# Optimization experiments

Hardware: AMD Instinct MI355X
Metric: run time of the kernel (lower is better)

## Reference

```python
import jax, jax.numpy as jnp
import numpy as np

N_QUBITS = 6
N_LAYERS = 2
QSVT_DEGREE = 3
DT_RANK = max(N_QUBITS // 2, 1)
OUT_DIM = 3 * N_QUBITS
PI = np.float32(np.pi)
DT_MIN, DT_MAX = 1e-3, 0.1
BATCH, SEQ = 256, 512


def _ry_mat(theta):
    c = jnp.cos(theta / 2)
    s = jnp.sin(theta / 2)
    row0 = jnp.stack([c, -s], axis=-1)
    row1 = jnp.stack([s, c], axis=-1)
    return jnp.stack([row0, row1], axis=-2).astype(jnp.complex64)


def _rz_mat(theta):
    e = jnp.exp(-0.5j * theta.astype(jnp.complex64))
    z = jnp.zeros_like(e)
    row0 = jnp.stack([e, z], axis=-1)
    row1 = jnp.stack([z, jnp.conj(e)], axis=-1)
    return jnp.stack([row0, row1], axis=-2)


def _rx_mat(theta):
    c = jnp.cos(theta / 2).astype(jnp.complex64)
    s = jnp.sin(theta / 2).astype(jnp.complex64)
    row0 = jnp.stack([c, -1j * s], axis=-1)
    row1 = jnp.stack([-1j * s, c], axis=-1)
    return jnp.stack([row0, row1], axis=-2)


def _apply1(state, mat, w):
    # state: (B, 2, ..., 2) tensor over N_QUBITS axes; mat: (2,2) or batched (B,2,2)
    state = jnp.moveaxis(state, 1 + w, -1)
    if mat.ndim == 3:
        state = jnp.einsum('bij,b...j->b...i', mat, state)
    else:
        state = jnp.einsum('ij,b...j->b...i', mat, state)
    return jnp.moveaxis(state, -1, 1 + w)


def _cnot(state, c, t):
    state = jnp.moveaxis(state, (1 + c, 1 + t), (-2, -1))
    state = state.at[..., 1, :].set(state[..., 1, ::-1])
    return jnp.moveaxis(state, (-2, -1), (1 + c, 1 + t))


def _crx(state, theta, c, t):
    state = jnp.moveaxis(state, (1 + c, 1 + t), (-2, -1))
    m = _rx_mat(theta)
    state = state.at[..., 1, :].set(jnp.einsum('ij,...j->...i', m, state[..., 1, :]))
    return jnp.moveaxis(state, (-2, -1), (1 + c, 1 + t))


def _circuit(h, x, dt, circuit_params, poly_coeffs, qsvt_params):
    """Batched statevector simulation of the selective QSVT + unified ansatz qnode."""
    n = N_QUBITS
    B = h.shape[0]
    state = jnp.zeros((B,) + (2,) * n, jnp.complex64)
    state = state.at[(slice(None),) + (0,) * n].set(1.0 + 0.0j)
    # 1) state encoding RY(h[t-1])
    for i in range(n):
        state = _apply1(state, _ry_mat(h[:, i]), i)
    # 2) Delta-modulated QSVT: RZ rotations + bidirectional CNOT ring per degree
    qidx = 0
    n_qp = n * QSVT_DEGREE
    for deg in range(QSVT_DEGREE + 1):
        coeff = poly_coeffs[deg]
        for i in range(n):
            if qidx < n_qp:
                ang = coeff * dt[:, i] * qsvt_params[qidx] * PI
                qidx += 1
            else:
                ang = coeff * dt[:, i] * PI
            state = _apply1(state, _rz_mat(ang), i)
        for i in range(n - 1):
            state = _cnot(state, i, i + 1)
        state = _cnot(state, n - 1, 0)
        for i in range(n - 1, 0, -1):
            state = _cnot(state, i, i - 1)
    # 3) unified variational ansatz
    p = 0
    for _ in range(N_LAYERS):
        for i in range(n):
            state = _apply1(state, _rx_mat(circuit_params[p]), i)
            state = _apply1(state, _ry_mat(circuit_params[p + 1]), i)
            state = _apply1(state, _rz_mat(circuit_params[p + 2]), i)
            p += 3
        for i in range(n):
            state = _crx(state, circuit_params[p], i, (i + 1) % n)
            p += 1
        for i in range(n - 1, -1, -1):
            state = _crx(state, circuit_params[p], i, (i - 1) % n)
            p += 1
    # 4) Delta-modulated input RY(x * dt)
    for i in range(n):
        state = _apply1(state, _ry_mat(x[:, i] * dt[:, i]), i)
    # 5) Pauli X/Y/Z expectation values per qubit
    xs, ys, zs = [], [], []
    for i in range(n):
        s = jnp.moveaxis(state, 1 + i, 1).reshape(B, 2, -1)
        z = jnp.sum(jnp.conj(s[:, 0]) * s[:, 1], axis=-1)
        xs.append(2.0 * jnp.real(z))
        ys.append(2.0 * jnp.imag(z))
        zs.append(jnp.sum(jnp.abs(s[:, 0]) ** 2 - jnp.abs(s[:, 1]) ** 2, axis=-1))
    return jnp.stack(xs + ys + zs, axis=-1).astype(jnp.float32)  # (B, 3n)


def setup_inputs() -> dict:
    key = jax.random.key(0)
    ks = jax.random.split(key, 8)
    angles = jax.random.uniform(ks[0], (BATCH, SEQ, N_QUBITS), jnp.float32) * PI
    Wx = jax.random.normal(ks[1], (DT_RANK + 2 * N_QUBITS, N_QUBITS), jnp.float32) / np.float32(np.sqrt(N_QUBITS))
    Wdt = jax.random.normal(ks[2], (N_QUBITS, DT_RANK), jnp.float32) / np.float32(np.sqrt(DT_RANK))
    dt = jnp.exp(jax.random.uniform(ks[3], (N_QUBITS,), jnp.float32) * np.float32(np.log(DT_MAX) - np.log(DT_MIN)) + np.float32(np.log(DT_MIN)))
    bdt = dt + jnp.log(-jnp.expm1(-dt))
    poly_coeffs = jax.random.normal(ks[4], (QSVT_DEGREE + 1,), jnp.float32) * 0.1
    qsvt_params = jax.random.normal(ks[5], (N_QUBITS * QSVT_DEGREE,), jnp.float32) * 0.1
    circuit_params = jax.random.normal(ks[6], (5 * N_QUBITS * N_LAYERS,), jnp.float32) * 0.1
    D = jnp.ones((OUT_DIM,), jnp.float32)
    Wc = jax.random.normal(ks[7], (OUT_DIM, N_QUBITS), jnp.float32) / np.float32(np.sqrt(N_QUBITS))
    return {"angles": angles, "Wx": Wx, "Wdt": Wdt, "bdt": bdt, "poly_coeffs": poly_coeffs, "qsvt_params": qsvt_params, "circuit_params": circuit_params, "D": D, "Wc": Wc}


def reference(angles, Wx, Wdt, bdt, poly_coeffs, qsvt_params, circuit_params, D, Wc):
    x_dbc = angles @ Wx.T  # (B,S, dt_rank + 2n)
    dt_raw = x_dbc[..., :DT_RANK]
    # B slice computed in the original but never used in forward
    C = x_dbc[..., DT_RANK + N_QUBITS:]
    dt_angles = jnp.tanh(jax.nn.softplus(dt_raw @ Wdt.T + bdt)) * PI  # (B,S,n)
    # quantum part is detached in the original (detach().cpu() before the qnode)
    sg = jax.lax.stop_gradient
    xs = (jnp.moveaxis(sg(angles), 1, 0), jnp.moveaxis(sg(dt_angles), 1, 0))
    cp, pc, qp = sg(circuit_params), sg(poly_coeffs), sg(qsvt_params)
    h0 = jnp.zeros((angles.shape[0], N_QUBITS), jnp.float32)

    def step(h, xt):
        x_t, dt_t = xt
        meas = _circuit(h, x_t, dt_t, cp, pc, qp)
        return meas[:, 2 * N_QUBITS:], meas  # carry = PauliZ block

    _, meas = jax.lax.scan(step, h0, xs)
    h_full = jnp.moveaxis(meas, 0, 1)  # (B,S,3n)
    return (C @ Wc.T) * h_full + D * jnp.concatenate([angles] * 3, axis=-1)
```

## Files before the change

### kernel.cpp

```cpp
#include <hip/hip_runtime.h>
#include <math.h>

#define BATCH 256
#define SEQ 512
#define SDS 54
#define PI_F 3.14159265358979323846f

template<int CTRL>
__device__ __forceinline__ float fdpp(float v) {
    return __int_as_float(__builtin_amdgcn_mov_dpp(__float_as_int(v), CTRL, 0xF, 0xF, true));
}
template<int L>
__device__ __forceinline__ float rdl(float v) {
    return __int_as_float(__builtin_amdgcn_readlane(__float_as_int(v), L));
}
__device__ __forceinline__ float rdlv(float v, int l) {
    return __int_as_float(__builtin_amdgcn_readlane(__float_as_int(v), l));
}
template<int M>
__device__ __forceinline__ float shxm(float v) {
    if constexpr (M == 1)       return fdpp<0xB1>(v);
    else if constexpr (M == 2)  return fdpp<0x4E>(v);
    else if constexpr (M == 8)  return fdpp<0x128>(v);
    else if constexpr (M == 32) return __shfl_xor(v, 32, 64);
    else return __int_as_float(__builtin_amdgcn_ds_swizzle(__float_as_int(v), (M << 10) | 0x1F));
}
__device__ __forceinline__ float redsum64(float v) {
    v += fdpp<0x128>(v);
    v += fdpp<0x124>(v);
    v += fdpp<0x122>(v);
    v += fdpp<0x121>(v);
    return (rdl<0>(v) + rdl<16>(v)) + (rdl<32>(v) + rdl<48>(v));
}
__device__ __forceinline__ float xorf(float v, int m) {
    return __int_as_float(__float_as_int(v) ^ m);
}
__device__ __forceinline__ void wg_barrier_lds() {
    __builtin_amdgcn_sched_barrier(0);
    __builtin_amdgcn_s_waitcnt(0xC07F);
    __builtin_amdgcn_s_barrier();
    __builtin_amdgcn_sched_barrier(0);
}
__device__ __forceinline__ int permf(int x) {
    const int cs[11] = {0,1,2,3,4,5,5,4,3,2,1};
    const int ts[11] = {1,2,3,4,5,0,4,3,2,1,0};
#pragma unroll
    for (int k = 10; k >= 0; k--) {
        int cb = (x >> (5 - cs[k])) & 1;
        x ^= cb << (5 - ts[k]);
    }
    return x;
}
__device__ __forceinline__ void cmul4(const float* c,
    float vr, float vi, float ar, float ai, float br, float bi, float cr, float ci,
    float& nr, float& ni) {
    nr = c[0]*vr - c[1]*vi + c[2]*ar - c[3]*ai + c[4]*br - c[5]*bi + c[6]*cr - c[7]*ci;
    ni = c[0]*vi + c[1]*vr + c[2]*ai + c[3]*ar + c[4]*bi + c[5]*br + c[6]*ci + c[7]*cr;
}
__device__ __forceinline__ void ringapply(const float* rc,
    float vr, float vi, float br, float bi, float cr, float ci, float dr, float di,
    float& nr, float& ni) {
    nr = rc[0]*vr - rc[1]*bi - rc[2]*ci + rc[3]*dr;
    ni = rc[0]*vi + rc[1]*br + rc[2]*cr + rc[3]*di;
}

__global__ __launch_bounds__(256) void prep_kernel(
    const float* __restrict__ angles, const float* __restrict__ Wx,
    const float* __restrict__ Wdt, const float* __restrict__ bdt,
    const float* __restrict__ D, const float* __restrict__ Wc,
    float* __restrict__ sd)
{
    int gid = blockIdx.x * blockDim.x + threadIdx.x;
    if (gid >= BATCH * SEQ) return;
    const float* a = angles + (size_t)gid * 6;
    float ang[6];
#pragma unroll
    for (int i = 0; i < 6; i++) ang[i] = a[i];
    float dtr[3];
#pragma unroll
    for (int r = 0; r < 3; r++) {
        float s = 0.f;
#pragma unroll
        for (int k = 0; k < 6; k++) s += ang[k] * Wx[r * 6 + k];
        dtr[r] = s;
    }
    float* rec = sd + (size_t)gid * SDS;
    float dtv[6];
#pragma unroll
    for (int i = 0; i < 6; i++) {
        float x = bdt[i];
#pragma unroll
        for (int r = 0; r < 3; r++) x += dtr[r] * Wdt[i * 3 + r];
        float sp = (x > 15.f) ? x : log1pf(expf(x));
        dtv[i] = tanhf(sp) * PI_F;
        rec[i] = dtv[i];
        float th = ang[i] * dtv[i];
        rec[6 + i]  = cosf(th);
        rec[12 + i] = sinf(th);
    }
    float C[6];
#pragma unroll
    for (int i = 0; i < 6; i++) {
        float s = 0.f;
#pragma unroll
        for (int k = 0; k < 6; k++) s += ang[k] * Wx[(9 + i) * 6 + k];
        C[i] = s;
    }
#pragma unroll
    for (int j = 0; j < 18; j++) {
        float s = 0.f;
#pragma unroll
        for (int i = 0; i < 6; i++) s += C[i] * Wc[j * 6 + i];
        rec[18 + j] = s;
        rec[36 + j] = D[j] * ang[j % 6];
    }
}

__global__ __launch_bounds__(64) void umat_kernel(const float* __restrict__ cp,
                                                  float2* __restrict__ um)
{
    const int lane = threadIdx.x;
    const int col = blockIdx.x;
    int bitv[6];
#pragma unroll
    for (int i = 0; i < 6; i++) bitv[i] = (lane >> (5 - i)) & 1;

    float qc[2][3][8], rc[2][6][4];
#pragma unroll
    for (int l = 0; l < 2; l++) {
        float g00r[6], g00i[6], g01r[6], g01i[6], g10r[6], g10i[6], g11r[6], g11i[6];
#pragma unroll
        for (int i = 0; i < 6; i++) {
            float ax = cp[l * 30 + i * 3 + 0];
            float ay = cp[l * 30 + i * 3 + 1];
            float az = cp[l * 30 + i * 3 + 2];
            float ca = cosf(0.5f * ax), sa = sinf(0.5f * ax);
            float cb = cosf(0.5f * ay), sb = sinf(0.5f * ay);
            float cg = cosf(0.5f * az), sg = sinf(0.5f * az);
            float m00r = cb * ca, m00i =  sb * sa;
            float m01r = -sb * ca, m01i = -cb * sa;
            float m10r =  sb * ca, m10i = -cb * sa;
            float m11r =  cb * ca, m11i = -sb * sa;
            g00r[i] = cg * m00r + sg * m00i; g00i[i] = cg * m00i - sg * m00r;
            g01r[i] = cg * m01r + sg * m01i; g01i[i] = cg * m01i - sg * m01r;
            g10r[i] = cg * m10r - sg * m10i; g10i[i] = cg * m10i + sg * m10r;
            g11r[i] = cg * m11r - sg * m11i; g11i[i] = cg * m11i + sg * m11r;
        }
#pragma unroll
        for (int pp = 0; pp < 3; pp++) {
            int aq = 2 * pp, bq = 2 * pp + 1;
            float dar = bitv[aq] ? g11r[aq] : g00r[aq], dai = bitv[aq] ? g11i[aq] : g00i[aq];
            float oar = bitv[aq] ? g10r[aq] : g01r[aq], oai = bitv[aq] ? g10i[aq] : g01i[aq];
            float dbr = bitv[bq] ? g11r[bq] : g00r[bq], dbi = bitv[bq] ? g11i[bq] : g00i[bq];
            float obr = bitv[bq] ? g10r[bq] : g01r[bq], obi = bitv[bq] ? g10i[bq] : g01i[bq];
            qc[l][pp][0] = dar * dbr - dai * dbi;  qc[l][pp][1] = dar * dbi + dai * dbr;
            qc[l][pp][2] = oar * dbr - oai * dbi;  qc[l][pp][3] = oar * dbi + oai * dbr;
            qc[l][pp][4] = dar * obr - dai * obi;  qc[l][pp][5] = dar * obi + dai * obr;
            qc[l][pp][6] = oar * obr - oai * obi;  qc[l][pp][7] = oar * obi + oai * obr;
        }
        const int Aq[6] = {0, 2, 4, 5, 3, 1};
        const int Bq[6] = {1, 3, 5, 4, 2, 0};
#pragma unroll
        for (int o = 0; o < 6; o++) {
            float tha = (o < 3) ? cp[l * 30 + 18 + 2 * o]     : cp[l * 30 + 24 + 2 * (o - 3)];
            float thb = (o < 3) ? cp[l * 30 + 18 + 2 * o + 1] : cp[l * 30 + 24 + 2 * (o - 3) + 1];
            float ca = cosf(0.5f * tha), sa = sinf(0.5f * tha);
            float cb = cosf(0.5f * thb), sb = sinf(0.5f * thb);
            int ba = bitv[Aq[o]], bb = bitv[Bq[o]];
            float mx0 = ba ? ca : 1.f, sae = ba ? sa : 0.f;
            float ny0 = bb ? cb : 1.f, sbe = bb ? sb : 0.f;
            rc[l][o][0] = ny0 * mx0; rc[l][o][1] = -ny0 * sae;
            rc[l][o][2] = -mx0 * sbe; rc[l][o][3] = -sae * sbe;
        }
    }

    float re = (lane == col) ? 1.f : 0.f;
    float im = 0.f;
    auto p1q = [&](int mi, int mj, const float* c) {
        float ar = __shfl_xor(re, mi, 64), ai = __shfl_xor(im, mi, 64);
        float br = __shfl_xor(re, mj, 64), bi = __shfl_xor(im, mj, 64);
        float cr = __shfl_xor(re, mi | mj, 64), ci = __shfl_xor(im, mi | mj, 64);
        float nr, ni;
        cmul4(c, re, im, ar, ai, br, bi, cr, ci, nr, ni);
        re = nr; im = ni;
    };
    auto rng = [&](int mb, int mc, const float* c) {
        float br = __shfl_xor(re, mb, 64), bi = __shfl_xor(im, mb, 64);
        float cr = __shfl_xor(re, mc, 64), ci = __shfl_xor(im, mc, 64);
        float dr = __shfl_xor(re, mb | mc, 64), di = __shfl_xor(im, mb | mc, 64);
        float nr, ni;
        ringapply(c, re, im, br, bi, cr, ci, dr, di, nr, ni);
        re = nr; im = ni;
    };
#pragma unroll
    for (int l = 0; l < 2; l++) {
        p1q(32, 16, qc[l][0]);
        p1q(8, 4, qc[l][1]);
        p1q(2, 1, qc[l][2]);
        rng(16, 8, rc[l][0]);
        rng(4, 2, rc[l][1]);
        rng(1, 32, rc[l][2]);
        rng(2, 4, rc[l][3]);
        rng(8, 16, rc[l][4]);
        rng(32, 1, rc[l][5]);
    }
    um[(size_t)lane * 64 + col] = make_float2(re, im);
}

__global__ __launch_bounds__(256, 1) void step_kernel(
    const float* __restrict__ sd, const float* __restrict__ pc,
    const float* __restrict__ qp, const float2* __restrict__ um,
    float* __restrict__ out)
{
    __shared__ float2 sPart[4][64];
    __shared__ __align__(16) float sZXY[20];
    const int tid = threadIdx.x;
    const int wave = tid >> 6;
    const int lane = tid & 63;
    const int b = blockIdx.x;

    int bitv[6];
#pragma unroll
    for (int i = 0; i < 6; i++) bitv[i] = (lane >> (5 - i)) & 1;
    int sflip[6];
#pragma unroll
    for (int q = 0; q < 6; q++) sflip[q] = bitv[q] ? (int)0x80000000 : 0;

    const int jbase = wave * 16;
    float2 row[16];
#pragma unroll
    for (int jj = 0; jj < 16; jj++) row[jj] = um[(size_t)lane * 64 + jbase + jj];

    float A[6], sel[6];
    {
        int x1 = permf(lane), x2 = permf(x1), x3 = permf(x2), x4 = permf(x3);
#pragma unroll
        for (int i = 0; i < 6; i++) {
            float u0 = pc[0] * PI_F * qp[0 * 6 + i];
            float u1 = pc[1] * PI_F * qp[1 * 6 + i];
            float u2 = pc[2] * PI_F * qp[2 * 6 + i];
            float u3 = pc[3] * PI_F;
            float t1 = ((x1 >> (5 - i)) & 1) ? 0.5f : -0.5f;
            float t2 = ((x2 >> (5 - i)) & 1) ? 0.5f : -0.5f;
            float t3 = ((x3 >> (5 - i)) & 1) ? 0.5f : -0.5f;
            float t4 = ((x4 >> (5 - i)) & 1) ? 0.5f : -0.5f;
            A[i] = u3 * t1 + u2 * t2 + u1 * t3 + u0 * t4;
            sel[i] = (float)((x4 >> (5 - i)) & 1);
        }
    }

    const float* sdb = sd + (size_t)b * SEQ * SDS;
    float* outb = out + (size_t)b * SEQ * 18;

    float h0 = 0.f, h1 = 0.f, h2 = 0.f, h3 = 0.f, h4 = 0.f, h5 = 0.f;

    float cd[18], nd[18];
#pragma unroll
    for (int k = 0; k < 18; k++) cd[k] = sdb[k];

    for (int t = 0; t < SEQ; t++) {
        const float* r  = sdb + (size_t)t * SDS;
        const float* rn = sdb + (size_t)((t + 1 < SEQ) ? t + 1 : t) * SDS;
#pragma unroll
        for (int k = 0; k < 18; k++) nd[k] = rn[k];

        float phi = A[0]*cd[0] + A[1]*cd[1] + A[2]*cd[2] + A[3]*cd[3] + A[4]*cd[4] + A[5]*cd[5];
        float sph, cph;
        __sincosf(phi, &sph, &cph);

        float ss0, cc0, ss1, cc1, ss2, cc2, ss3, cc3, ss4, cc4, ss5, cc5;
        __sincosf(0.5f * h0, &ss0, &cc0);
        __sincosf(0.5f * h1, &ss1, &cc1);
        __sincosf(0.5f * h2, &ss2, &cc2);
        __sincosf(0.5f * h3, &ss3, &cc3);
        __sincosf(0.5f * h4, &ss4, &cc4);
        __sincosf(0.5f * h5, &ss5, &cc5);
        float f0 = fmaf(sel[0], ss0 - cc0, cc0);
        float f1 = fmaf(sel[1], ss1 - cc1, cc1);
        float f2 = fmaf(sel[2], ss2 - cc2, cc2);
        float f3 = fmaf(sel[3], ss3 - cc3, cc3);
        float f4 = fmaf(sel[4], ss4 - cc4, cc4);
        float f5 = fmaf(sel[5], ss5 - cc5, cc5);
        float prod = ((f0 * f1) * (f2 * f3)) * (f4 * f5);
        float pr = prod * cph, pi = prod * sph;

        float ar0 = 0.f, ai0 = 0.f, ar1 = 0.f, ai1 = 0.f;
#pragma unroll
        for (int jj = 0; jj < 16; jj += 2) {
            float sr0 = rdlv(pr, jbase + jj);
            float si0 = rdlv(pi, jbase + jj);
            float sr1 = rdlv(pr, jbase + jj + 1);
            float si1 = rdlv(pi, jbase + jj + 1);
            ar0 = fmaf(row[jj].x, sr0, ar0);
            ar0 = fmaf(-row[jj].y, si0, ar0);
            ai0 = fmaf(row[jj].x, si0, ai0);
            ai0 = fmaf(row[jj].y, sr0, ai0);
            ar1 = fmaf(row[jj + 1].x, sr1, ar1);
            ar1 = fmaf(-row[jj + 1].y, si1, ar1);
            ai1 = fmaf(row[jj + 1].x, si1, ai1);
            ai1 = fmaf(row[jj + 1].y, sr1, ai1);
        }
        sPart[wave][lane] = make_float2(ar0 + ar1, ai0 + ai1);
        wg_barrier_lds();
        float2 q0v = sPart[0][lane], q1v = sPart[1][lane];
        float2 q2v = sPart[2][lane], q3v = sPart[3][lane];
        float re = (q0v.x + q1v.x) + (q2v.x + q3v.x);
        float im = (q0v.y + q1v.y) + (q2v.y + q3v.y);

        if (wave == 0) {
            float p = re * re + im * im;
            float Z0 = redsum64(xorf(p, sflip[0]));
            float Z1 = redsum64(xorf(p, sflip[1]));
            float Z2 = redsum64(xorf(p, sflip[2]));
            float Z3 = redsum64(xorf(p, sflip[3]));
            float Z4 = redsum64(xorf(p, sflip[4]));
            float Z5 = redsum64(xorf(p, sflip[5]));
            if (lane == 0) {
                sZXY[0] = Z0; sZXY[1] = Z1; sZXY[2] = Z2;
                sZXY[3] = Z3; sZXY[4] = Z4; sZXY[5] = Z5;
            }
        } else if (wave == 1) {
            float g0r = shxm<32>(re), g0i = shxm<32>(im);
            float g1r = shxm<16>(re), g1i = shxm<16>(im);
            float X0 = redsum64(re * g0r + im * g0i);
            float X1 = redsum64(re * g1r + im * g1i);
            float Y0 = redsum64(xorf(re * g0i - im * g0r, sflip[0]));
            float Y1 = redsum64(xorf(re * g1i - im * g1r, sflip[1]));
            if (lane == 0) { sZXY[6] = X0; sZXY[7] = X1; sZXY[12] = Y0; sZXY[13] = Y1; }
        } else if (wave == 2) {
            float g2r = shxm<8>(re), g2i = shxm<8>(im);
            float g3r = shxm<4>(re), g3i = shxm<4>(im);
            float X2 = redsum64(re * g2r + im * g2i);
            float X3 = redsum64(re * g3r + im * g3i);
            float Y2 = redsum64(xorf(re * g2i - im * g2r, sflip[2]));
            float Y3 = redsum64(xorf(re * g3i - im * g3r, sflip[3]));
            if (lane == 0) { sZXY[8] = X2; sZXY[9] = X3; sZXY[14] = Y2; sZXY[15] = Y3; }
        } else {
            float g4r = shxm<2>(re), g4i = shxm<2>(im);
            float g5r = shxm<1>(re), g5i = shxm<1>(im);
            float X4 = redsum64(re * g4r + im * g4i);
            float X5 = redsum64(re * g5r + im * g5i);
            float Y4 = redsum64(xorf(re * g4i - im * g4r, sflip[4]));
            float Y5 = redsum64(xorf(re * g5i - im * g5r, sflip[5]));
            if (lane == 0) { sZXY[10] = X4; sZXY[11] = X5; sZXY[16] = Y4; sZXY[17] = Y5; }
        }
        wg_barrier_lds();

        float4 v0 = ((const float4*)sZXY)[0];
        float4 v1 = ((const float4*)sZXY)[1];
        float4 v2 = ((const float4*)sZXY)[2];
        float Zv[6] = {v0.x, v0.y, v0.z, v0.w, v1.x, v1.y};
        float Xv[6] = {v1.z, v1.w, v2.x, v2.y, v2.z, v2.w};
        h0 = cd[6]  * Zv[0] - cd[12] * Xv[0];
        h1 = cd[7]  * Zv[1] - cd[13] * Xv[1];
        h2 = cd[8]  * Zv[2] - cd[14] * Xv[2];
        h3 = cd[9]  * Zv[3] - cd[15] * Xv[3];
        h4 = cd[10] * Zv[4] - cd[16] * Xv[4];
        h5 = cd[11] * Zv[5] - cd[17] * Xv[5];

        if (wave == 0 && lane == 0) {
            float* o = outb + (size_t)t * 18;
            float hh[6] = {h0, h1, h2, h3, h4, h5};
#pragma unroll
            for (int q = 0; q < 6; q++) o[12 + q] = fmaf(r[30 + q], hh[q], r[48 + q]);
        }
        if (wave == 3 && lane == 0) {
            float* o = outb + (size_t)t * 18;
#pragma unroll
            for (int q = 0; q < 6; q++) {
                float px = cd[6 + q] * Xv[q] + cd[12 + q] * Zv[q];
                o[q]     = fmaf(r[18 + q], px, r[36 + q]);
                o[6 + q] = fmaf(r[24 + q], sZXY[12 + q], r[42 + q]);
            }
        }

#pragma unroll
        for (int k = 0; k < 18; k++) cd[k] = nd[k];
    }
}

extern "C" void kernel_launch(void* const* d_in, const int* in_sizes, int n_in,
                              void* d_out, int out_size, void* d_ws, size_t ws_size,
                              hipStream_t stream) {
    const float* angles = (const float*)d_in[0];
    const float* Wx     = (const float*)d_in[1];
    const float* Wdt    = (const float*)d_in[2];
    const float* bdt    = (const float*)d_in[3];
    const float* pc     = (const float*)d_in[4];
    const float* qp     = (const float*)d_in[5];
    const float* cp     = (const float*)d_in[6];
    const float* D      = (const float*)d_in[7];
    const float* Wc     = (const float*)d_in[8];
    float* sd  = (float*)d_ws;
    float2* um = (float2*)(sd + (size_t)BATCH * SEQ * SDS);
    float* out = (float*)d_out;

    umat_kernel<<<64, 64, 0, stream>>>(cp, um);
    prep_kernel<<<(BATCH * SEQ) / 256, 256, 0, stream>>>(angles, Wx, Wdt, bdt, D, Wc, sd);
    step_kernel<<<BATCH, 256, 0, stream>>>(sd, pc, qp, um, out);
}
```

Baseline: 707.1 us.

## Split step kernel across 8 waves and move output epilogue to a post kernel

Each block now runs 8 waves instead of 4. Each wave handles 8 matrix columns, and the X/Y/Z reductions are spread so that each wave does one qubit's X/Y pair or three Z values. The per-step output arithmetic is moved out of the serial time loop: raw Z/X/Y are written to the output buffer, and a separate post_kernel applies the Wc/D scaling. The loop is also unrolled by two with double-buffered float2 loads of the step data. The aim is a shorter serial critical path per timestep, at the cost of more barrier participants and an extra pass over the output.

```diff
diff --git a/kernel.cpp b/kernel.cpp
--- a/kernel.cpp
+++ b/kernel.cpp
@@ -207,13 +207,13 @@
     um[(size_t)lane * 64 + col] = make_float2(re, im);
 }
 
-__global__ __launch_bounds__(256, 1) void step_kernel(
+__global__ __launch_bounds__(512, 1) void step_kernel(
     const float* __restrict__ sd, const float* __restrict__ pc,
     const float* __restrict__ qp, const float2* __restrict__ um,
     float* __restrict__ out)
 {
-    __shared__ float2 sPart[4][64];
-    __shared__ __align__(16) float sZXY[20];
+    __shared__ float2 sPart[8][64];
+    __shared__ __align__(16) float sZX[12];
     const int tid = threadIdx.x;
     const int wave = tid >> 6;
     const int lane = tid & 63;
@@ -226,10 +226,10 @@
 #pragma unroll
     for (int q = 0; q < 6; q++) sflip[q] = bitv[q] ? (int)0x80000000 : 0;
 
-    const int jbase = wave * 16;
-    float2 row[16];
-#pragma unroll
-    for (int jj = 0; jj < 16; jj++) row[jj] = um[(size_t)lane * 64 + jbase + jj];
+    const int jbase = wave * 8;
+    float2 row[8];
+#pragma unroll
+    for (int jj = 0; jj < 8; jj++) row[jj] = um[(size_t)lane * 64 + jbase + jj];
 
     float A[6], sel[6];
     {
@@ -254,17 +254,29 @@
 
     float h0 = 0.f, h1 = 0.f, h2 = 0.f, h3 = 0.f, h4 = 0.f, h5 = 0.f;
 
-    float cd[18], nd[18];
-#pragma unroll
-    for (int k = 0; k < 18; k++) cd[k] = sdb[k];
-
-    for (int t = 0; t < SEQ; t++) {
-        const float* r  = sdb + (size_t)t * SDS;
-        const float* rn = sdb + (size_t)((t + 1 < SEQ) ? t + 1 : t) * SDS;
-#pragma unroll
-        for (int k = 0; k < 18; k++) nd[k] = rn[k];
-
-        float phi = A[0]*cd[0] + A[1]*cd[1] + A[2]*cd[2] + A[3]*cd[3] + A[4]*cd[4] + A[5]*cd[5];
+    float bufA[18], bufB[18];
+    {
+        const float2* p2 = (const float2*)sdb;
+#pragma unroll
+        for (int k = 0; k < 9; k++) {
+            float2 v = p2[k];
+            bufA[2 * k] = v.x; bufA[2 * k + 1] = v.y;
+        }
+    }
+
+    auto body = [&](float (&cur)[18], float (&nxt)[18], int t) {
+        {
+            int tn = (t + 1 < SEQ) ? t + 1 : t;
+            const float2* rn2 = (const float2*)(sdb + (size_t)tn * SDS);
+#pragma unroll
+            for (int k = 0; k < 9; k++) {
+                float2 v = rn2[k];
+                nxt[2 * k] = v.x; nxt[2 * k + 1] = v.y;
+            }
+        }
+
+        float phi = A[0]*cur[0] + A[1]*cur[1] + A[2]*cur[2]
+                  + A[3]*cur[3] + A[4]*cur[4] + A[5]*cur[5];
         float sph, cph;
         __sincosf(phi, &sph, &cph);
 
@@ -286,7 +298,7 @@
 
         float ar0 = 0.f, ai0 = 0.f, ar1 = 0.f, ai1 = 0.f;
 #pragma unroll
-        for (int jj = 0; jj < 16; jj += 2) {
+        for (int jj = 0; jj < 8; jj += 2) {
             float sr0 = rdlv(pr, jbase + jj);
             float si0 = rdlv(pi, jbase + jj);
             float sr1 = rdlv(pr, jbase + jj + 1);
@@ -302,81 +314,102 @@
         }
         sPart[wave][lane] = make_float2(ar0 + ar1, ai0 + ai1);
         wg_barrier_lds();
-        float2 q0v = sPart[0][lane], q1v = sPart[1][lane];
-        float2 q2v = sPart[2][lane], q3v = sPart[3][lane];
-        float re = (q0v.x + q1v.x) + (q2v.x + q3v.x);
-        float im = (q0v.y + q1v.y) + (q2v.y + q3v.y);
-
+        float2 p0 = sPart[0][lane], p1 = sPart[1][lane];
+        float2 p2 = sPart[2][lane], p3 = sPart[3][lane];
+        float2 p4 = sPart[4][lane], p5 = sPart[5][lane];
+        float2 p6 = sPart[6][lane], p7 = sPart[7][lane];
+        float re = ((p0.x + p1.x) + (p2.x + p3.x)) + ((p4.x + p5.x) + (p6.x + p7.x));
+        float im = ((p0.y + p1.y) + (p2.y + p3.y)) + ((p4.y + p5.y) + (p6.y + p7.y));
+
+        float* o = outb + (size_t)t * 18;
+        auto xy = [&](int q, int sf, float gr, float gi) {
+            float X = redsum64(re * gr + im * gi);
+            float Y = redsum64(xorf(re * gi - im * gr, sf));
+            if (lane == 0) { sZX[6 + q] = X; o[6 + q] = X; o[12 + q] = Y; }
+        };
         if (wave == 0) {
             float p = re * re + im * im;
             float Z0 = redsum64(xorf(p, sflip[0]));
             float Z1 = redsum64(xorf(p, sflip[1]));
             float Z2 = redsum64(xorf(p, sflip[2]));
+            if (lane == 0) {
+                sZX[0] = Z0; sZX[1] = Z1; sZX[2] = Z2;
+                o[0] = Z0; o[1] = Z1; o[2] = Z2;
+            }
+        } else if (wave == 1) {
+            float p = re * re + im * im;
             float Z3 = redsum64(xorf(p, sflip[3]));
             float Z4 = redsum64(xorf(p, sflip[4]));
             float Z5 = redsum64(xorf(p, sflip[5]));
             if (lane == 0) {
-                sZXY[0] = Z0; sZXY[1] = Z1; sZXY[2] = Z2;
-                sZXY[3] = Z3; sZXY[4] = Z4; sZXY[5] = Z5;
+                sZX[3] = Z3; sZX[4] = Z4; sZX[5] = Z5;
+                o[3] = Z3; o[4] = Z4; o[5] = Z5;
             }
-        } else if (wave == 1) {
-            float g0r = shxm<32>(re), g0i = shxm<32>(im);
-            float g1r = shxm<16>(re), g1i = shxm<16>(im);
-            float X0 = redsum64(re * g0r + im * g0i);
-            float X1 = redsum64(re * g1r + im * g1i);
-            float Y0 = redsum64(xorf(re * g0i - im * g0r, sflip[0]));
-            float Y1 = redsum64(xorf(re * g1i - im * g1r, sflip[1]));
-            if (lane == 0) { sZXY[6] = X0; sZXY[7] = X1; sZXY[12] = Y0; sZXY[13] = Y1; }
-        } else if (wave == 2) {
-            float g2r = shxm<8>(re), g2i = shxm<8>(im);
-            float g3r = shxm<4>(re), g3i = shxm<4>(im);
-            float X2 = redsum64(re * g2r + im * g2i);
-            float X3 = redsum64(re * g3r + im * g3i);
-            float Y2 = redsum64(xorf(re * g2i - im * g2r, sflip[2]));
-            float Y3 = redsum64(xorf(re * g3i - im * g3r, sflip[3]));
-            if (lane == 0) { sZXY[8] = X2; sZXY[9] = X3; sZXY[14] = Y2; sZXY[15] = Y3; }
-        } else {
-            float g4r = shxm<2>(re), g4i = shxm<2>(im);
-            float g5r = shxm<1>(re), g5i = shxm<1>(im);
-            float X4 = redsum64(re * g4r + im * g4i);
-            float X5 = redsum64(re * g5r + im * g5i);
-            float Y4 = redsum64(xorf(re * g4i - im * g4r, sflip[4]));
-            float Y5 = redsum64(xorf(re * g5i - im * g5r, sflip[5]));
-            if (lane == 0) { sZXY[10] = X4; sZXY[11] = X5; sZXY[16] = Y4; sZXY[17] = Y5; }
-        }
+        } else if (wave == 2) { xy(0, sflip[0], shxm<32>(re), shxm<32>(im)); }
+          else if (wave == 3) { xy(1, sflip[1], shxm<16>(re), shxm<16>(im)); }
+          else if (wave == 4) { xy(2, sflip[2], shxm<8>(re),  shxm<8>(im));  }
+          else if (wave == 5) { xy(3, sflip[3], shxm<4>(re),  shxm<4>(im));  }
+          else if (wave == 6) { xy(4, sflip[4], shxm<2>(re),  shxm<2>(im));  }
+          else                { xy(5, sflip[5], shxm<1>(re),  shxm<1>(im));  }
         wg_barrier_lds();
 
-        float4 v0 = ((const float4*)sZXY)[0];
-        float4 v1 = ((const float4*)sZXY)[1];
-        float4 v2 = ((const float4*)sZXY)[2];
-        float Zv[6] = {v0.x, v0.y, v0.z, v0.w, v1.x, v1.y};
-        float Xv[6] = {v1.z, v1.w, v2.x, v2.y, v2.z, v2.w};
-        h0 = cd[6]  * Zv[0] - cd[12] * Xv[0];
-        h1 = cd[7]  * Zv[1] - cd[13] * Xv[1];
-        h2 = cd[8]  * Zv[2] - cd[14] * Xv[2];
-        h3 = cd[9]  * Zv[3] - cd[15] * Xv[3];
-        h4 = cd[10] * Zv[4] - cd[16] * Xv[4];
-        h5 = cd[11] * Zv[5] - cd[17] * Xv[5];
-
-        if (wave == 0 && lane == 0) {
-            float* o = outb + (size_t)t * 18;
-            float hh[6] = {h0, h1, h2, h3, h4, h5};
-#pragma unroll
-            for (int q = 0; q < 6; q++) o[12 + q] = fmaf(r[30 + q], hh[q], r[48 + q]);
-        }
-        if (wave == 3 && lane == 0) {
-            float* o = outb + (size_t)t * 18;
-#pragma unroll
-            for (int q = 0; q < 6; q++) {
-                float px = cd[6 + q] * Xv[q] + cd[12 + q] * Zv[q];
-                o[q]     = fmaf(r[18 + q], px, r[36 + q]);
-                o[6 + q] = fmaf(r[24 + q], sZXY[12 + q], r[42 + q]);
-            }
-        }
-
-#pragma unroll
-        for (int k = 0; k < 18; k++) cd[k] = nd[k];
-    }
+        float4 v0 = ((const float4*)sZX)[0];
+        float4 v1 = ((const float4*)sZX)[1];
+        float4 v2 = ((const float4*)sZX)[2];
+        h0 = cur[6]  * v0.x - cur[12] * v1.z;
+        h1 = cur[7]  * v0.y - cur[13] * v1.w;
+        h2 = cur[8]  * v0.z - cur[14] * v2.x;
+        h3 = cur[9]  * v0.w - cur[15] * v2.y;
+        h4 = cur[10] * v1.x - cur[16] * v2.z;
+        h5 = cur[11] * v1.y - cur[17] * v2.w;
+    };
+
+    for (int t = 0; t < SEQ; t += 2) {
+        body(bufA, bufB, t);
+        body(bufB, bufA, t + 1);
+    }
+}
+
+__global__ __launch_bounds__(256) void post_kernel(
+    const float* __restrict__ sd, float* __restrict__ out)
+{
+    int gid = blockIdx.x * blockDim.x + threadIdx.x;
+    if (gid >= BATCH * SEQ) return;
+    const float* rec = sd + (size_t)gid * SDS;
+    float* o = out + (size_t)gid * 18;
+
+    float zxy[18];
+    {
+        const float2* o2 = (const float2*)o;
+#pragma unroll
+        for (int k = 0; k < 9; k++) {
+            float2 v = o2[k];
+            zxy[2 * k] = v.x; zxy[2 * k + 1] = v.y;
+        }
+    }
+    float r[54];
+    {
+        const float2* r2 = (const float2*)rec;
+#pragma unroll
+        for (int k = 3; k < 27; k++) {
+            float2 v = r2[k];
+            r[2 * k] = v.x; r[2 * k + 1] = v.y;
+        }
+    }
+    float res[18];
+#pragma unroll
+    for (int q = 0; q < 6; q++) {
+        float Z = zxy[q], X = zxy[6 + q], Y = zxy[12 + q];
+        float c = r[6 + q], s = r[12 + q];
+        float px = c * X + s * Z;
+        float hq = c * Z - s * X;
+        res[q]      = fmaf(r[18 + q], px, r[36 + q]);
+        res[6 + q]  = fmaf(r[24 + q], Y,  r[42 + q]);
+        res[12 + q] = fmaf(r[30 + q], hq, r[48 + q]);
+    }
+    float2* ow = (float2*)o;
+#pragma unroll
+    for (int k = 0; k < 9; k++) ow[k] = make_float2(res[2 * k], res[2 * k + 1]);
 }
 
 extern "C" void kernel_launch(void* const* d_in, const int* in_sizes, int n_in,
@@ -397,5 +430,6 @@
 
     umat_kernel<<<64, 64, 0, stream>>>(cp, um);
     prep_kernel<<<(BATCH * SEQ) / 256, 256, 0, stream>>>(angles, Wx, Wdt, bdt, D, Wc, sd);
-    step_kernel<<<BATCH, 256, 0, stream>>>(sd, pc, qp, um, out);
-}
+    step_kernel<<<BATCH, 512, 0, stream>>>(sd, pc, qp, um, out);
+    post_kernel<<<(BATCH * SEQ) / 256, 256, 0, stream>>>(sd, out);
+}
```

Result: no change. 720.9 us (+1.9%).
